# Kernel optimization log

Hardware: AMD Instinct MI355X
Metric: run time of the kernel (lower is better)

## Reference

```python
import jax, jax.numpy as jnp
import numpy as np

N_QUBITS = 10
Q_DEPTH = 6
MAX_LAYERS = 15
DIM = 2 ** N_QUBITS


def _apply_1q(s, U, w):
    # s: (B, 2^n) real statevector (circuit uses only H/RY/CNOT, all real).
    # Wire 0 is the most-significant bit (PennyLane convention).
    a, b = 2 ** w, 2 ** (N_QUBITS - 1 - w)
    s = s.reshape(-1, a, 2, b)
    if U.ndim == 2:  # gate shared across batch
        s = jnp.einsum('ij,Bajb->Baib', U, s)
    else:            # per-sample gate, U: (B,2,2)
        s = jnp.einsum('Bij,Bajb->Baib', U, s)
    return s.reshape(-1, DIM)


def _apply_cnot(s, c, t):
    # CNOT, control c < target t
    s = s.reshape(-1, 2 ** c, 2, 2 ** (t - c - 1), 2, 2 ** (N_QUBITS - 1 - t))
    s = jnp.stack([s[:, :, 0], jnp.flip(s[:, :, 1], axis=3)], axis=2)
    return s.reshape(-1, DIM)


def _ry(theta):
    # RY(theta) = [[cos t/2, -sin t/2], [sin t/2, cos t/2]]; theta scalar or (B,)
    c, si = jnp.cos(theta / 2.0), jnp.sin(theta / 2.0)
    return jnp.stack([jnp.stack([c, -si], -1), jnp.stack([si, c], -1)], -2)


def _quantum_net(q_in, q_params):
    # q_in: (B, n_qubits) rotation angles; q_params: (max_layers*n_qubits,)
    B = q_in.shape[0]
    qw = q_params.reshape(MAX_LAYERS, N_QUBITS)
    s = jnp.zeros((B, DIM), q_in.dtype).at[:, 0].set(1.0)  # |0...0>
    H = jnp.array([[1.0, 1.0], [1.0, -1.0]], q_in.dtype) / jnp.sqrt(jnp.asarray(2.0, q_in.dtype))
    for w in range(N_QUBITS):
        s = _apply_1q(s, H, w)
    for w in range(N_QUBITS):
        s = _apply_1q(s, _ry(q_in[:, w]), w)
    for k in range(Q_DEPTH):
        for i in range(0, N_QUBITS - 1, 2):
            s = _apply_cnot(s, i, i + 1)
        for i in range(1, N_QUBITS - 1, 2):
            s = _apply_cnot(s, i, i + 1)
        for w in range(N_QUBITS):
            s = _apply_1q(s, _ry(qw[k + 1, w]), w)
    probs = s * s
    # <Z_w> = P(bit_w = 0) - P(bit_w = 1)
    z = []
    for w in range(N_QUBITS):
        p = probs.reshape(-1, 2 ** w, 2, 2 ** (N_QUBITS - 1 - w)).sum(axis=(1, 3))
        z.append(p[:, 0] - p[:, 1])
    return jnp.stack(z, axis=1)  # (B, n_qubits)


def setup_inputs() -> dict:
    key = jax.random.key(0)
    ks = jax.random.split(key, 6)
    B, F, NQ, NC = 8192, 512, N_QUBITS, 2
    q_delta = 0.01
    return {
        'input_features': jax.random.normal(ks[0], (B, F), jnp.float32),
        'W_pre': jax.random.normal(ks[1], (NQ, F), jnp.float32) / np.sqrt(F),
        'b_pre': jnp.zeros((NQ,), jnp.float32),
        'q_params': q_delta * jax.random.normal(ks[2], (MAX_LAYERS * NQ,), jnp.float32),
        'W_post': jax.random.normal(ks[3], (NC, NQ), jnp.float32) / np.sqrt(NQ),
        'b_post': jnp.zeros((NC,), jnp.float32),
    }


def reference(input_features, W_pre, b_pre, q_params, W_post, b_post):
    pre_out = input_features @ W_pre.T + b_pre          # (B, n_qubits)
    q_in = jnp.tanh(pre_out) * (np.pi / 2.0)            # scale to [-pi/2, pi/2]
    q_out = _quantum_net(q_in, q_params)                # (B, n_qubits) PauliZ expvals
    return q_out @ W_post.T + b_post                    # (B, n_classes)
```

## Files before the change

kernel.cpp:

```cpp
#include <hip/hip_runtime.h>
#include <math.h>


#define NQ   10
#define NREG 16
#define DIM  1024

typedef _Float16 f16;
typedef _Float16 f16x8 __attribute__((ext_vector_type(8)));
typedef float    f32x4 __attribute__((ext_vector_type(4)));

template<int BB>
__device__ __forceinline__ void ry_lane(float (&s)[NREG], int lane, float c, float si) {
    float sgn = ((lane >> BB) & 1) ? si : -si;
    #pragma unroll
    for (int r = 0; r < NREG; ++r) {
        float o = __shfl_xor(s[r], 1 << BB);
        s[r] = fmaf(sgn, o, c * s[r]);
    }
}
template<int P>
__device__ __forceinline__ void ry_reg(float (&s)[NREG], float c, float si) {
    const int m = 1 << P;
    #pragma unroll
    for (int r = 0; r < NREG; ++r) {
        if ((r & m) == 0) {
            float a = s[r], b = s[r + m];
            s[r]     = fmaf(c, a, -si * b);
            s[r + m] = fmaf(si, a,  c * b);
        }
    }
}
__device__ __forceinline__ void cnot_5_6(float (&s)[NREG], int lane) {
    bool sel = (lane & 1) != 0;
    #pragma unroll
    for (int r = 0; r < 8; ++r) {
        float a = s[r], b = s[r + 8];
        s[r]     = sel ? b : a;
        s[r + 8] = sel ? a : b;
    }
}
template<int PC, int PT>
__device__ __forceinline__ void cnot_reg(float (&s)[NREG]) {
    #pragma unroll
    for (int r = 0; r < NREG; ++r) {
        if (((r >> PC) & 1) && !((r >> PT) & 1)) {
            float t = s[r];
            s[r] = s[r ^ (1 << PT)];
            s[r ^ (1 << PT)] = t;
        }
    }
}
__device__ __forceinline__ void perm_even(float (&s)[NREG], int lane) {
    int src = lane ^ (((((lane >> 5) & 1) << 4)) | ((((lane >> 3) & 1) << 2)) | (((lane >> 1) & 1)));
    #pragma unroll
    for (int r = 0; r < NREG; ++r) s[r] = __shfl(s[r], src);
}
__device__ __forceinline__ void perm_odd(float (&s)[NREG], int lane) {
    int src = lane ^ (((((lane >> 4) & 1) << 3)) | ((((lane >> 2) & 1) << 1)));
    #pragma unroll
    for (int r = 0; r < NREG; ++r) s[r] = __shfl(s[r], src);
}

#define APPLY_RY_ALL(CARR, SARR, BASE)                                        \
    { float c_, s_;                                                           \
      c_=__shfl(CARR,(BASE)+0); s_=__shfl(SARR,(BASE)+0); ry_lane<5>(s,lane,c_,s_); \
      c_=__shfl(CARR,(BASE)+1); s_=__shfl(SARR,(BASE)+1); ry_lane<4>(s,lane,c_,s_); \
      c_=__shfl(CARR,(BASE)+2); s_=__shfl(SARR,(BASE)+2); ry_lane<3>(s,lane,c_,s_); \
      c_=__shfl(CARR,(BASE)+3); s_=__shfl(SARR,(BASE)+3); ry_lane<2>(s,lane,c_,s_); \
      c_=__shfl(CARR,(BASE)+4); s_=__shfl(SARR,(BASE)+4); ry_lane<1>(s,lane,c_,s_); \
      c_=__shfl(CARR,(BASE)+5); s_=__shfl(SARR,(BASE)+5); ry_lane<0>(s,lane,c_,s_); \
      c_=__shfl(CARR,(BASE)+6); s_=__shfl(SARR,(BASE)+6); ry_reg<3>(s,c_,s_);       \
      c_=__shfl(CARR,(BASE)+7); s_=__shfl(SARR,(BASE)+7); ry_reg<2>(s,c_,s_);       \
      c_=__shfl(CARR,(BASE)+8); s_=__shfl(SARR,(BASE)+8); ry_reg<1>(s,c_,s_);       \
      c_=__shfl(CARR,(BASE)+9); s_=__shfl(SARR,(BASE)+9); ry_reg<0>(s,c_,s_); }

__device__ __forceinline__ void async16(const void* g, void* l) {
    __builtin_amdgcn_global_load_lds(
        (const __attribute__((address_space(1))) void*)g,
        (__attribute__((address_space(3))) void*)l, 16, 0, 0);
}

__global__ __launch_bounds__(256) void ka_prepare(
    const float* __restrict__ X, const float* __restrict__ Wpre,
    const float* __restrict__ bpre, const float* __restrict__ qp,
    f16* __restrict__ psi0, f16* __restrict__ Arm, int B)
{
    const int tid = threadIdx.x, lane = tid & 63, wv = tid >> 6;

    for (int it = 0; it < 4; ++it) {
        int sample = blockIdx.x * 16 + wv * 4 + it;
        if (sample >= B) break;
        const float* xrow = X + (size_t)sample * 512;
        float4 x0 = ((const float4*)xrow)[lane];
        float4 x1 = ((const float4*)xrow)[64 + lane];
        float acc[NQ];
        #pragma unroll
        for (int q = 0; q < NQ; ++q) {
            const float* wr = Wpre + q * 512;
            float4 w0 = ((const float4*)wr)[lane];
            float4 w1 = ((const float4*)wr)[64 + lane];
            float a = x0.x * w0.x;
            a = fmaf(x0.y, w0.y, a); a = fmaf(x0.z, w0.z, a); a = fmaf(x0.w, w0.w, a);
            a = fmaf(x1.x, w1.x, a); a = fmaf(x1.y, w1.y, a);
            a = fmaf(x1.z, w1.z, a); a = fmaf(x1.w, w1.w, a);
            acc[q] = a;
        }
        #pragma unroll
        for (int q = 0; q < NQ; ++q) {
            float v = acc[q];
            #pragma unroll
            for (int d = 32; d >= 1; d >>= 1) v += __shfl_xor(v, d);
            acc[q] = v;
        }
        float pre = acc[0];
        #pragma unroll
        for (int q = 1; q < NQ; ++q) pre = (lane == q) ? acc[q] : pre;
        float c45 = 0.0f, s45 = 0.0f;
        if (lane < NQ) {
            float th = tanhf(pre + bpre[lane]) * 1.5707963267948966f;
            sincosf(0.5f * th + 0.7853981633974483f, &s45, &c45);
        }
        float lv = 1.0f;
        #pragma unroll
        for (int w = 0; w < 6; ++w) {
            float f0 = __shfl(c45, w), f1 = __shfl(s45, w);
            lv *= ((lane >> (5 - w)) & 1) ? f1 : f0;
        }
        float c6 = __shfl(c45, 6), s6 = __shfl(s45, 6);
        float c7 = __shfl(c45, 7), s7 = __shfl(s45, 7);
        float c8 = __shfl(c45, 8), s8 = __shfl(s45, 8);
        float c9 = __shfl(c45, 9), s9 = __shfl(s45, 9);
        float g01[4] = {c6 * c7, c6 * s7, s6 * c7, s6 * s7};
        float g23[4] = {c8 * c9, c8 * s9, s8 * c9, s8 * s9};
        union { f16 h[16]; float4 v[2]; } u;
        #pragma unroll
        for (int r = 0; r < NREG; ++r)
            u.h[r] = (f16)(lv * g01[r >> 2] * g23[r & 3]);
        float4* dst = (float4*)((char*)psi0 + (size_t)sample * 2048 + lane * 32);
        dst[0] = u.v[0];
        dst[1] = u.v[1];
    }

    if (wv < 2) {
        int row = blockIdx.x * 2 + wv;
        if (row < DIM) {
            float cw = 1.0f, swn = 0.0f;
            if (lane < 60) {
                float s_, c_;
                sincosf(0.5f * qp[10 + lane], &s_, &c_);
                cw = c_; swn = -s_;
            }
            float s[NREG];
            int srcLane = row >> 4, srcReg = row & 15;
            #pragma unroll
            for (int r = 0; r < NREG; ++r)
                s[r] = (lane == srcLane && r == srcReg) ? 1.0f : 0.0f;
            for (int kk = 6; kk >= 1; --kk) {
                APPLY_RY_ALL(cw, swn, (kk - 1) * 10);
                perm_odd(s, lane);
                cnot_5_6(s, lane);
                cnot_reg<2, 1>(s);
                perm_even(s, lane);
                cnot_reg<3, 2>(s);
                cnot_reg<1, 0>(s);
            }
            union { f16 h[16]; float4 v[2]; } u;
            #pragma unroll
            for (int r = 0; r < NREG; ++r) u.h[r] = (f16)s[r];
            float4* dst = (float4*)((char*)Arm + (size_t)row * 2048 + lane * 32);
            dst[0] = u.v[0];
            dst[1] = u.v[1];
        }
    }
}

__global__ __launch_bounds__(256, 2) void kb_gemm_measure(
    const f16* __restrict__ psi0, const f16* __restrict__ Arm,
    float* __restrict__ zpart)
{
    __shared__ __align__(16) char smem[32768];
    const int tid = threadIdx.x, lane = tid & 63, wv = tid >> 6;

    const int mB = blockIdx.x & 63, nB = blockIdx.x >> 6;
    const size_t tM = (size_t)mB * 128, tN = (size_t)nB * 128;
    f16* As = (f16*)smem;
    f16* Bs = (f16*)(smem + 16384);
    const int wm = (wv >> 1) * 64, wn = (wv & 1) * 64;

    f32x4 acc[4][4] = {};

    const f16* ga[4]; const f16* gb[4]; int ldso[4];
    #pragma unroll
    for (int p = 0; p < 4; ++p) {
        int slot = p * 256 + tid;
        int row = slot >> 3, gp = slot & 7, g = gp ^ (row & 7);
        ga[p] = psi0 + (tM + row) * 1024 + g * 8;
        gb[p] = Arm  + (tN + row) * 1024 + g * 8;
        ldso[p] = slot * 16;
    }

    for (int kt = 0; kt < 1024; kt += 64) {
        __syncthreads();
        #pragma unroll
        for (int p = 0; p < 4; ++p) async16(ga[p] + kt, (char*)As + ldso[p]);
        #pragma unroll
        for (int p = 0; p < 4; ++p) async16(gb[p] + kt, (char*)Bs + ldso[p]);
        __syncthreads();
        #pragma unroll
        for (int ks = 0; ks < 2; ++ks) {
            f16x8 af[4], bf[4];
            const int gpb = ks * 4 + (lane >> 4);
            const int gpx = gpb ^ (lane & 7);
            #pragma unroll
            for (int i = 0; i < 4; ++i) {
                int rowA = wm + i * 16 + (lane & 15);
                af[i] = *(const f16x8*)(As + rowA * 64 + gpx * 8);
            }
            #pragma unroll
            for (int j = 0; j < 4; ++j) {
                int rowB = wn + j * 16 + (lane & 15);
                bf[j] = *(const f16x8*)(Bs + rowB * 64 + gpx * 8);
            }
            #pragma unroll
            for (int i = 0; i < 4; ++i)
                #pragma unroll
                for (int j = 0; j < 4; ++j)
                    acc[i][j] = __builtin_amdgcn_mfma_f32_16x16x32_f16(af[i], bf[j], acc[i][j], 0, 0, 0);
        }
    }

    __syncthreads();
    float* zb = (float*)smem + (wn ? 1280 : 0);
    const float sg0 = (nB & 4) ? -1.0f : 1.0f;
    const float sg1 = (nB & 2) ? -1.0f : 1.0f;
    const float sg2 = (nB & 1) ? -1.0f : 1.0f;
    const float sg3 = wn ? -1.0f : 1.0f;

    #pragma unroll
    for (int i = 0; i < 4; ++i) {
        #pragma unroll
        for (int t = 0; t < 4; ++t) {
            float p0 = acc[i][0][t] * acc[i][0][t];
            float p1 = acc[i][1][t] * acc[i][1][t];
            float p2 = acc[i][2][t] * acc[i][2][t];
            float p3 = acc[i][3][t] * acc[i][3][t];
            float t0  = (p0 + p1) + (p2 + p3);
            float tw5 = (p0 - p1) + (p2 - p3);
            float tw4 = (p0 + p1) - (p2 + p3);
            float s1 = __shfl_xor(t0, 1);
            float Av = t0 + s1;
            float Bv = (lane & 1) ? s1 - t0 : t0 - s1;
            float sA = __shfl_xor(Av, 2), sB = __shfl_xor(Bv, 2);
            float AP = Av + sA;
            float AM = (lane & 2) ? sA - Av : Av - sA;
            float BP = Bv + sB;
            float sAP = __shfl_xor(AP, 4), sAM = __shfl_xor(AM, 4), sBP = __shfl_xor(BP, 4);
            float APP = AP + sAP;
            float APM = (lane & 4) ? sAP - AP : AP - sAP;
            float AMP = AM + sAM;
            float BPP = BP + sBP;
            float a1 = __shfl_xor(APP, 8), a2 = __shfl_xor(APM, 8);
            float a3 = __shfl_xor(AMP, 8), a4 = __shfl_xor(BPP, 8);
            float T0 = APP + a1;
            float S6 = (lane & 8) ? a1 - APP : APP - a1;
            float S7 = APM + a2;
            float S8 = AMP + a3;
            float S9 = BPP + a4;
            float T5 = tw5, T4 = tw4;
            T5 += __shfl_xor(T5, 1); T5 += __shfl_xor(T5, 2);
            T5 += __shfl_xor(T5, 4); T5 += __shfl_xor(T5, 8);
            T4 += __shfl_xor(T4, 1); T4 += __shfl_xor(T4, 2);
            T4 += __shfl_xor(T4, 4); T4 += __shfl_xor(T4, 8);
            if ((lane & 15) == 0) {
                int row = wm + i * 16 + (lane >> 4) * 4 + t;
                float* d = zb + row * 10;
                d[0] = sg0 * T0; d[1] = sg1 * T0; d[2] = sg2 * T0; d[3] = sg3 * T0;
                d[4] = T4; d[5] = T5;
                d[6] = S6; d[7] = S7; d[8] = S8; d[9] = S9;
            }
        }
    }
    __syncthreads();
    float* zall = (float*)smem;
    for (int idx = tid; idx < 1280; idx += 256) {
        float v = zall[idx] + zall[1280 + idx];
        int row = idx / 10, w = idx - row * 10;
        zpart[((size_t)nB * 8192 + tM + row) * 10 + w] = v;
    }
}

__global__ __launch_bounds__(256) void kc_post(
    const float* __restrict__ zpart, const float* __restrict__ Wpost,
    const float* __restrict__ bpost, float* __restrict__ out, int B)
{
    int gid = blockIdx.x * 256 + threadIdx.x;
    if (gid >= B) return;
    float z[NQ] = {};
    #pragma unroll
    for (int nb = 0; nb < 8; ++nb) {
        const float* zp = zpart + ((size_t)nb * 8192 + gid) * 10;
        #pragma unroll
        for (int w = 0; w < NQ; ++w) z[w] += zp[w];
    }
    float o0 = bpost[0], o1 = bpost[1];
    #pragma unroll
    for (int w = 0; w < NQ; ++w) {
        o0 = fmaf(z[w], Wpost[w], o0);
        o1 = fmaf(z[w], Wpost[NQ + w], o1);
    }
    out[(size_t)gid * 2 + 0] = o0;
    out[(size_t)gid * 2 + 1] = o1;
}

template<int BC, int BT>
__device__ __forceinline__ void cnot_lane(float (&s)[NREG], int lane) {
    int src = ((lane >> BC) & 1) ? (lane ^ (1 << BT)) : lane;
    #pragma unroll
    for (int r = 0; r < NREG; ++r) s[r] = __shfl(s[r], src);
}

__global__ __launch_bounds__(256) void hybrid_head_fallback(
    const float* __restrict__ X, const float* __restrict__ Wpre,
    const float* __restrict__ bpre, const float* __restrict__ qp,
    const float* __restrict__ Wpost, const float* __restrict__ bpost,
    float* __restrict__ out, int B)
{
    const int lane = threadIdx.x & 63;
    const int wave = threadIdx.x >> 6;
    const int sample = blockIdx.x * 4 + wave;
    if (sample >= B) return;

    const float* xrow = X + (size_t)sample * 512;
    float4 x0 = ((const float4*)xrow)[lane];
    float4 x1 = ((const float4*)xrow)[64 + lane];
    float acc[NQ];
    #pragma unroll
    for (int q = 0; q < NQ; ++q) {
        const float* wr = Wpre + q * 512;
        float4 w0 = ((const float4*)wr)[lane];
        float4 w1 = ((const float4*)wr)[64 + lane];
        float a = x0.x * w0.x;
        a = fmaf(x0.y, w0.y, a); a = fmaf(x0.z, w0.z, a); a = fmaf(x0.w, w0.w, a);
        a = fmaf(x1.x, w1.x, a); a = fmaf(x1.y, w1.y, a);
        a = fmaf(x1.z, w1.z, a); a = fmaf(x1.w, w1.w, a);
        acc[q] = a;
    }
    #pragma unroll
    for (int q = 0; q < NQ; ++q) {
        float v = acc[q];
        #pragma unroll
        for (int d = 32; d >= 1; d >>= 1) v += __shfl_xor(v, d);
        acc[q] = v;
    }
    float pre = acc[0];
    #pragma unroll
    for (int q = 1; q < NQ; ++q) pre = (lane == q) ? acc[q] : pre;
    float cth = 1.0f, sth = 0.0f;
    if (lane < NQ) {
        float th = tanhf(pre + bpre[lane]) * 1.5707963267948966f;
        sincosf(0.5f * th, &sth, &cth);
    }
    float cw = 1.0f, sw = 0.0f;
    if (lane < 60) sincosf(0.5f * qp[10 + lane], &sw, &cw);

    float s[NREG];
    #pragma unroll
    for (int r = 0; r < NREG; ++r) s[r] = 0.03125f;
    APPLY_RY_ALL(cth, sth, 0);
    for (int k = 0; k < 6; ++k) {
        perm_even(s, lane);
        cnot_reg<3, 2>(s);
        cnot_reg<1, 0>(s);
        perm_odd(s, lane);
        cnot_5_6(s, lane);
        cnot_reg<2, 1>(s);
        APPLY_RY_ALL(cw, sw, k * 10);
    }
    float p[NREG], tot = 0.0f;
    #pragma unroll
    for (int r = 0; r < NREG; ++r) { p[r] = s[r] * s[r]; tot += p[r]; }
    float z[NQ];
    #pragma unroll
    for (int w = 0; w < 6; ++w) z[w] = ((lane >> (5 - w)) & 1) ? -tot : tot;
    z[6] = z[7] = z[8] = z[9] = 0.0f;
    #pragma unroll
    for (int r = 0; r < NREG; ++r) {
        z[6] += ((r >> 3) & 1) ? -p[r] : p[r];
        z[7] += ((r >> 2) & 1) ? -p[r] : p[r];
        z[8] += ((r >> 1) & 1) ? -p[r] : p[r];
        z[9] += ((r >> 0) & 1) ? -p[r] : p[r];
    }
    #pragma unroll
    for (int w = 0; w < NQ; ++w) {
        float v = z[w];
        #pragma unroll
        for (int d = 32; d >= 1; d >>= 1) v += __shfl_xor(v, d);
        z[w] = v;
    }
    if (lane < 2) {
        const float* wp = Wpost + lane * NQ;
        float o = bpost[lane];
        #pragma unroll
        for (int w = 0; w < NQ; ++w) o = fmaf(z[w], wp[w], o);
        out[(size_t)sample * 2 + lane] = o;
    }
}

extern "C" void kernel_launch(void* const* d_in, const int* in_sizes, int n_in,
                              void* d_out, int out_size, void* d_ws, size_t ws_size,
                              hipStream_t stream) {
    const float* X     = (const float*)d_in[0];
    const float* Wpre  = (const float*)d_in[1];
    const float* bpre  = (const float*)d_in[2];
    const float* qp    = (const float*)d_in[3];
    const float* Wpost = (const float*)d_in[4];
    const float* bpost = (const float*)d_in[5];
    float* out = (float*)d_out;
    int B = in_sizes[0] / 512;

    size_t psi0_b  = (size_t)B * DIM * sizeof(f16);
    size_t arm_b   = (size_t)DIM * DIM * sizeof(f16);
    size_t zpart_b = (size_t)8 * 8192 * 10 * sizeof(float);
    size_t need = psi0_b + arm_b + zpart_b;

    if (B != 8192 || ws_size < need) {
        hipLaunchKernelGGL(hybrid_head_fallback, dim3((B + 3) / 4), dim3(256), 0, stream,
                           X, Wpre, bpre, qp, Wpost, bpost, out, B);
        return;
    }

    char* ws = (char*)d_ws;
    f16*   psi0  = (f16*)ws;
    f16*   Arm   = (f16*)(ws + psi0_b);
    float* zpart = (float*)(ws + psi0_b + arm_b);

    hipLaunchKernelGGL(ka_prepare, dim3(512), dim3(256), 0, stream,
                       X, Wpre, bpre, qp, psi0, Arm, B);
    hipLaunchKernelGGL(kb_gemm_measure, dim3(512), dim3(256), 0, stream,
                       psi0, Arm, zpart);
    hipLaunchKernelGGL(kc_post, dim3(32), dim3(256), 0, stream,
                       zpart, Wpost, bpost, out, B);
}
```

Measured before the change: 126.2 us.

## Halve GEMM M-tile to 64 rows and reduce partials with atomics

The GEMM-measure kernel now uses 64x128 tiles instead of 128x128. That doubles the grid to 1024 blocks, cuts LDS to 24KB and raises the occupancy hint to 4 blocks per CU. Per-block Z-expectation partials are accumulated directly into a single zeroed buffer with atomicAdd instead of writing 8 separate slabs, so the post kernel reads one row per sample. The prepare kernel zeroes that buffer. The change trades more A/B refetch per FLOP and atomic contention for better latency hiding and less partial-sum traffic.

```diff
diff --git a/kernel.cpp b/kernel.cpp
--- a/kernel.cpp
+++ b/kernel.cpp
@@ -84,9 +84,14 @@
 __global__ __launch_bounds__(256) void ka_prepare(
     const float* __restrict__ X, const float* __restrict__ Wpre,
     const float* __restrict__ bpre, const float* __restrict__ qp,
-    f16* __restrict__ psi0, f16* __restrict__ Arm, int B)
+    f16* __restrict__ psi0, f16* __restrict__ Arm, float* __restrict__ z, int B)
 {
     const int tid = threadIdx.x, lane = tid & 63, wv = tid >> 6;
+
+    {
+        int idx = blockIdx.x * 256 + tid;
+        if (idx < 8192 * NQ) z[idx] = 0.0f;
+    }
 
     for (int it = 0; it < 4; ++it) {
         int sample = blockIdx.x * 16 + wv * 4 + it;
@@ -175,45 +180,52 @@
     }
 }
 
-__global__ __launch_bounds__(256, 2) void kb_gemm_measure(
+__global__ __launch_bounds__(256, 4) void kb_gemm_measure(
     const f16* __restrict__ psi0, const f16* __restrict__ Arm,
-    float* __restrict__ zpart)
+    float* __restrict__ z)
 {
-    __shared__ __align__(16) char smem[32768];
+    __shared__ __align__(16) char smem[24576];
     const int tid = threadIdx.x, lane = tid & 63, wv = tid >> 6;
 
-    const int mB = blockIdx.x & 63, nB = blockIdx.x >> 6;
-    const size_t tM = (size_t)mB * 128, tN = (size_t)nB * 128;
+    const int mB = blockIdx.x & 127, nB = blockIdx.x >> 7;
+    const size_t tM = (size_t)mB * 64, tN = (size_t)nB * 128;
     f16* As = (f16*)smem;
-    f16* Bs = (f16*)(smem + 16384);
-    const int wm = (wv >> 1) * 64, wn = (wv & 1) * 64;
-
-    f32x4 acc[4][4] = {};
-
-    const f16* ga[4]; const f16* gb[4]; int ldso[4];
+    f16* Bs = (f16*)(smem + 8192);
+    const int wm = (wv >> 1) * 32, wn = (wv & 1) * 64;
+
+    f32x4 acc[2][4] = {};
+
+    const f16* ga[2]; int ldsoA[2];
+    #pragma unroll
+    for (int p = 0; p < 2; ++p) {
+        int slot = p * 256 + tid;
+        int row = slot >> 3, gp = slot & 7, g = gp ^ (row & 7);
+        ga[p] = psi0 + (tM + row) * 1024 + g * 8;
+        ldsoA[p] = slot * 16;
+    }
+    const f16* gb[4]; int ldsoB[4];
     #pragma unroll
     for (int p = 0; p < 4; ++p) {
         int slot = p * 256 + tid;
         int row = slot >> 3, gp = slot & 7, g = gp ^ (row & 7);
-        ga[p] = psi0 + (tM + row) * 1024 + g * 8;
-        gb[p] = Arm  + (tN + row) * 1024 + g * 8;
-        ldso[p] = slot * 16;
+        gb[p] = Arm + (tN + row) * 1024 + g * 8;
+        ldsoB[p] = slot * 16;
     }
 
     for (int kt = 0; kt < 1024; kt += 64) {
         __syncthreads();
         #pragma unroll
-        for (int p = 0; p < 4; ++p) async16(ga[p] + kt, (char*)As + ldso[p]);
-        #pragma unroll
-        for (int p = 0; p < 4; ++p) async16(gb[p] + kt, (char*)Bs + ldso[p]);
+        for (int p = 0; p < 2; ++p) async16(ga[p] + kt, (char*)As + ldsoA[p]);
+        #pragma unroll
+        for (int p = 0; p < 4; ++p) async16(gb[p] + kt, (char*)Bs + ldsoB[p]);
         __syncthreads();
         #pragma unroll
         for (int ks = 0; ks < 2; ++ks) {
-            f16x8 af[4], bf[4];
+            f16x8 af[2], bf[4];
             const int gpb = ks * 4 + (lane >> 4);
             const int gpx = gpb ^ (lane & 7);
             #pragma unroll
-            for (int i = 0; i < 4; ++i) {
+            for (int i = 0; i < 2; ++i) {
                 int rowA = wm + i * 16 + (lane & 15);
                 af[i] = *(const f16x8*)(As + rowA * 64 + gpx * 8);
             }
@@ -223,7 +235,7 @@
                 bf[j] = *(const f16x8*)(Bs + rowB * 64 + gpx * 8);
             }
             #pragma unroll
-            for (int i = 0; i < 4; ++i)
+            for (int i = 0; i < 2; ++i)
                 #pragma unroll
                 for (int j = 0; j < 4; ++j)
                     acc[i][j] = __builtin_amdgcn_mfma_f32_16x16x32_f16(af[i], bf[j], acc[i][j], 0, 0, 0);
@@ -231,14 +243,14 @@
     }
 
     __syncthreads();
-    float* zb = (float*)smem + (wn ? 1280 : 0);
+    float* zb = (float*)smem + (wn ? 640 : 0);
     const float sg0 = (nB & 4) ? -1.0f : 1.0f;
     const float sg1 = (nB & 2) ? -1.0f : 1.0f;
     const float sg2 = (nB & 1) ? -1.0f : 1.0f;
     const float sg3 = wn ? -1.0f : 1.0f;
 
     #pragma unroll
-    for (int i = 0; i < 4; ++i) {
+    for (int i = 0; i < 2; ++i) {
         #pragma unroll
         for (int t = 0; t < 4; ++t) {
             float p0 = acc[i][0][t] * acc[i][0][t];
@@ -283,31 +295,26 @@
     }
     __syncthreads();
     float* zall = (float*)smem;
-    for (int idx = tid; idx < 1280; idx += 256) {
-        float v = zall[idx] + zall[1280 + idx];
+    for (int idx = tid; idx < 640; idx += 256) {
+        float v = zall[idx] + zall[640 + idx];
         int row = idx / 10, w = idx - row * 10;
-        zpart[((size_t)nB * 8192 + tM + row) * 10 + w] = v;
+        atomicAdd(&z[((size_t)tM + row) * 10 + w], v);
     }
 }
 
 __global__ __launch_bounds__(256) void kc_post(
-    const float* __restrict__ zpart, const float* __restrict__ Wpost,
+    const float* __restrict__ z, const float* __restrict__ Wpost,
     const float* __restrict__ bpost, float* __restrict__ out, int B)
 {
     int gid = blockIdx.x * 256 + threadIdx.x;
     if (gid >= B) return;
-    float z[NQ] = {};
-    #pragma unroll
-    for (int nb = 0; nb < 8; ++nb) {
-        const float* zp = zpart + ((size_t)nb * 8192 + gid) * 10;
-        #pragma unroll
-        for (int w = 0; w < NQ; ++w) z[w] += zp[w];
-    }
+    const float* zp = z + (size_t)gid * NQ;
     float o0 = bpost[0], o1 = bpost[1];
     #pragma unroll
     for (int w = 0; w < NQ; ++w) {
-        o0 = fmaf(z[w], Wpost[w], o0);
-        o1 = fmaf(z[w], Wpost[NQ + w], o1);
+        float zw = zp[w];
+        o0 = fmaf(zw, Wpost[w], o0);
+        o1 = fmaf(zw, Wpost[NQ + w], o1);
     }
     out[(size_t)gid * 2 + 0] = o0;
     out[(size_t)gid * 2 + 1] = o1;
@@ -419,10 +426,10 @@
     float* out = (float*)d_out;
     int B = in_sizes[0] / 512;
 
-    size_t psi0_b  = (size_t)B * DIM * sizeof(f16);
-    size_t arm_b   = (size_t)DIM * DIM * sizeof(f16);
-    size_t zpart_b = (size_t)8 * 8192 * 10 * sizeof(float);
-    size_t need = psi0_b + arm_b + zpart_b;
+    size_t psi0_b = (size_t)B * DIM * sizeof(f16);
+    size_t arm_b  = (size_t)DIM * DIM * sizeof(f16);
+    size_t z_b    = (size_t)B * NQ * sizeof(float);
+    size_t need = psi0_b + arm_b + z_b;
 
     if (B != 8192 || ws_size < need) {
         hipLaunchKernelGGL(hybrid_head_fallback, dim3((B + 3) / 4), dim3(256), 0, stream,
@@ -431,14 +438,14 @@
     }
 
     char* ws = (char*)d_ws;
-    f16*   psi0  = (f16*)ws;
-    f16*   Arm   = (f16*)(ws + psi0_b);
-    float* zpart = (float*)(ws + psi0_b + arm_b);
+    f16*   psi0 = (f16*)ws;
+    f16*   Arm  = (f16*)(ws + psi0_b);
+    float* z    = (float*)(ws + psi0_b + arm_b);
 
     hipLaunchKernelGGL(ka_prepare, dim3(512), dim3(256), 0, stream,
-                       X, Wpre, bpre, qp, psi0, Arm, B);
-    hipLaunchKernelGGL(kb_gemm_measure, dim3(512), dim3(256), 0, stream,
-                       psi0, Arm, zpart);
+                       X, Wpre, bpre, qp, psi0, Arm, z, B);
+    hipLaunchKernelGGL(kb_gemm_measure, dim3(1024), dim3(256), 0, stream,
+                       psi0, Arm, z);
     hipLaunchKernelGGL(kc_post, dim3(32), dim3(256), 0, stream,
-                       zpart, Wpost, bpost, out, B);
-}
+                       z, Wpost, bpost, out, B);
+}
```

Result: no change. 124.9 us (-1.0%).
